# Kernel optimization log

Hardware: AMD Instinct MI355X
Metric: run time of the kernel (lower is better)

Reference implementation:

```python
import jax, jax.numpy as jnp
import numpy as np

B, S, E, WIN = 8, 2048, 512, 11  # batch, seq_len, emb_dim, window_size (odd)
PAD_VAL = 0.0  # padding_idx used as constant pad value in F.pad


def setup_inputs() -> dict:
    key = jax.random.key(0)
    k1, k2, k3 = jax.random.split(key, 3)
    x = jax.random.normal(k1, (B, S, E), dtype=jnp.float32)
    lim = 1.0 / np.sqrt(E * WIN)  # torch Linear default init bound
    # One independent Linear per timestep (deepcopy clones): stacked weights/bias
    W = jax.random.uniform(k2, (S, WIN, WIN * E), minval=-lim, maxval=lim, dtype=jnp.float32)
    b = jax.random.uniform(k3, (S, WIN), minval=-lim, maxval=lim, dtype=jnp.float32)
    return {"x": x, "W": W, "b": b}


def reference(x, W, b):
    ww = WIN // 2
    # pad sequence dim on both sides with padding_idx
    padded = jnp.pad(x, ((0, 0), (ww, ww), (0, 0)), constant_values=PAD_VAL)  # [B, S+2ww, E]
    # gather all sliding windows at once: windows[b,t,j,:] = padded[b, t+j, :]
    idx = jnp.arange(S)[:, None] + jnp.arange(WIN)[None, :]
    windows = padded[:, idx, :]
    flat = windows.reshape(B, S, WIN * E)                     # flattened window per position
    gates = jax.nn.sigmoid(jnp.einsum('bsf,swf->bsw', flat, W) + b)
    # gate * embeddings, sum over window, tanh
    score = jnp.einsum('bsw,bswe->bse', gates, windows)       # [B, S, E]
    return jnp.tanh(score)
```

## Files before the change

kernel.cpp:

```cpp
#include <hip/hip_runtime.h>
#include <math.h>

#define B_    8
#define S_    2048
#define E_    512
#define WIN_  11
#define WW    5
#define F4C   1408
#define E4C   128
#define PSTR  (B_ * WIN_)
#define HC_W  704
#define HC_X  512

template <int CTRL, int RMASK>
__device__ __forceinline__ float dpp_add(float v) {
    int sh = __builtin_amdgcn_update_dpp(0, __float_as_int(v),
                                         CTRL, RMASK, 0xF, true);
    return v + __int_as_float(sh);
}
__device__ __forceinline__ float wave_sum63(float v) {
    v = dpp_add<0x111, 0xF>(v);
    v = dpp_add<0x112, 0xF>(v);
    v = dpp_add<0x114, 0xF>(v);
    v = dpp_add<0x118, 0xF>(v);
    v = dpp_add<0x142, 0xA>(v);
    v = dpp_add<0x143, 0xC>(v);
    return v;
}

__device__ __forceinline__ float tanh_fast(float v) {
    const float e = __expf(v + v);
    return 1.f - 2.f / (e + 1.f);
}

__global__ __launch_bounds__(256)
void win_attn_fused(const float* __restrict__ x,
                    const float* __restrict__ W,
                    const float* __restrict__ bias,
                    float* __restrict__ out)
{
    const int bid  = blockIdx.x;
    const int s    = (bid & 7) * (S_ / 8) + (bid >> 3);
    const int tid  = threadIdx.x;
    const int wid  = tid >> 6;
    const int lane = tid & 63;

    const float4* __restrict__ X4 = reinterpret_cast<const float4*>(x);
    const float4* __restrict__ Ws = reinterpret_cast<const float4*>(W)
                                    + (size_t)s * (WIN_ * F4C);

    __shared__ float4 Wb[2][HC_W];
    __shared__ float4 xb[2][HC_X];
    __shared__ float gates[PSTR];

    const int w0   = wid * 3;
    const int wcnt = (wid == 3) ? 2 : 3;

    auto STAGE = [&](int buf, int c) {
        const int wp  = c >> 1;
        const int h   = c & 1;
        const int row = s - WW + wp;
        #pragma unroll
        for (int j = 0; j < 3; ++j) {
            const int m = j * 256 + tid;
            if (j < 2 || tid < 192) {
                const int w  = m >> 6;
                const int el = m & 63;
                const float4* src = Ws + (size_t)w * F4C + wp * E4C + h * 64 + el;
                __builtin_amdgcn_global_load_lds(
                    (const __attribute__((address_space(1))) void*)src,
                    (__attribute__((address_space(3))) void*)&Wb[buf][m],
                    16, 0, 0);
            }
        }
        #pragma unroll
        for (int j = 0; j < 2; ++j) {
            const int n  = j * 256 + tid;
            const int b  = n >> 6;
            const int el = n & 63;
            const float4* src = X4 + ((size_t)b * S_ + row) * E4C + h * 64 + el;
            __builtin_amdgcn_global_load_lds(
                (const __attribute__((address_space(1))) void*)src,
                (__attribute__((address_space(3))) void*)&xb[buf][n],
                16, 0, 0);
        }
    };

    float acc[B_][3];
    #pragma unroll
    for (int b = 0; b < B_; ++b)
        #pragma unroll
        for (int j = 0; j < 3; ++j) acc[b][j] = 0.f;

    const int wpLo = (s >= WW) ? 0 : (WW - s);
    const int wpHi = (WIN_ < S_ + WW - s) ? WIN_ : (S_ + WW - s);
    const int cLo  = 2 * wpLo, cHi = 2 * wpHi;

    STAGE(0, cLo);
    int cur = 0;

    #pragma unroll 1
    for (int c = cLo; c < cHi; ++c) {
        const bool more = (c + 1 < cHi);
        if (more) STAGE(cur ^ 1, c + 1);

        if (more) {
            if (wid < 3) asm volatile("s_waitcnt vmcnt(5)" ::: "memory");
            else         asm volatile("s_waitcnt vmcnt(4)" ::: "memory");
        } else {
            asm volatile("s_waitcnt vmcnt(0)" ::: "memory");
        }
        __builtin_amdgcn_s_barrier();
        __builtin_amdgcn_sched_barrier(0);

        float4 wv[3];
        #pragma unroll
        for (int j = 0; j < 3; ++j)
            if (j < wcnt) wv[j] = Wb[cur][(w0 + j) * 64 + lane];

        float4 xv[B_];
        #pragma unroll
        for (int b = 0; b < B_; ++b) xv[b] = xb[cur][b * 64 + lane];

        #pragma unroll
        for (int b = 0; b < B_; ++b)
            #pragma unroll
            for (int j = 0; j < 3; ++j)
                if (j < wcnt) {
                    float a = acc[b][j];
                    a = fmaf(xv[b].x, wv[j].x, a);
                    a = fmaf(xv[b].y, wv[j].y, a);
                    a = fmaf(xv[b].z, wv[j].z, a);
                    a = fmaf(xv[b].w, wv[j].w, a);
                    acc[b][j] = a;
                }

        __builtin_amdgcn_s_barrier();
        cur ^= 1;
    }

    #pragma unroll
    for (int b = 0; b < B_; ++b)
        #pragma unroll
        for (int j = 0; j < 3; ++j)
            if (j < wcnt) acc[b][j] = wave_sum63(acc[b][j]);

    if (lane == 63) {
        #pragma unroll
        for (int b = 0; b < B_; ++b)
            #pragma unroll
            for (int j = 0; j < 3; ++j)
                if (j < wcnt) gates[b * WIN_ + w0 + j] = acc[b][j];
    }
    __syncthreads();

    if (tid < PSTR) {
        const int w = tid % WIN_;
        const float v = gates[tid] + bias[s * WIN_ + w];
        gates[tid] = 1.f / (1.f + __expf(-v));
    }
    __syncthreads();

    float4* __restrict__ OUT4 = reinterpret_cast<float4*>(out);
    #pragma unroll
    for (int it = 0; it < 4; ++it) {
        const int i  = tid + (it << 8);
        const int b  = i >> 7;
        const int e4 = i & 127;
        float4 sc = make_float4(0.f, 0.f, 0.f, 0.f);
        #pragma unroll
        for (int w = 0; w < WIN_; ++w) {
            const int r = s - WW + w;
            if (r >= 0 && r < S_) {
                const float g   = gates[b * WIN_ + w];
                const float4 xv = X4[((size_t)b * S_ + r) * E4C + e4];
                sc.x = fmaf(g, xv.x, sc.x);
                sc.y = fmaf(g, xv.y, sc.y);
                sc.z = fmaf(g, xv.z, sc.z);
                sc.w = fmaf(g, xv.w, sc.w);
            }
        }
        float4 o;
        o.x = tanh_fast(sc.x);
        o.y = tanh_fast(sc.y);
        o.z = tanh_fast(sc.z);
        o.w = tanh_fast(sc.w);
        OUT4[((size_t)b * S_ + s) * E4C + e4] = o;
    }
}

extern "C" void kernel_launch(void* const* d_in, const int* in_sizes, int n_in,
                              void* d_out, int out_size, void* d_ws, size_t ws_size,
                              hipStream_t stream)
{
    const float* x    = (const float*)d_in[0];
    const float* W    = (const float*)d_in[1];
    const float* bias = (const float*)d_in[2];
    float* out        = (float*)d_out;

    win_attn_fused<<<dim3(S_), dim3(256), 0, stream>>>(x, W, bias, out);
}
```

Before: 146.6 us.

## Process two timesteps per block to share staged window rows of x

Each block now handles two adjacent sequence positions. It iterates over the 12 input rows covering both windows and loads each x row into LDS once, using it against both timesteps' weight slices. This halves the grid and cuts repeated x staging. In exchange it drops the double-buffered asynchronous pipeline with fine-grained vmcnt waits, and uses plain __syncthreads between loads and compute. That can expose load latency on the dominant W stream, whose traffic is unchanged.

```diff
diff --git a/kernel.cpp b/kernel.cpp
--- a/kernel.cpp
+++ b/kernel.cpp
@@ -8,9 +8,9 @@
 #define WW    5
 #define F4C   1408
 #define E4C   128
+#define G_    2
+#define NBLK  (S_ / G_)
 #define PSTR  (B_ * WIN_)
-#define HC_W  704
-#define HC_X  512
 
 template <int CTRL, int RMASK>
 __device__ __forceinline__ float dpp_add(float v) {
@@ -40,152 +40,189 @@
                     float* __restrict__ out)
 {
     const int bid  = blockIdx.x;
-    const int s    = (bid & 7) * (S_ / 8) + (bid >> 3);
+    const int sb   = (bid & 7) * (NBLK / 8) + (bid >> 3);
+    const int s0   = sb * G_;
     const int tid  = threadIdx.x;
     const int wid  = tid >> 6;
     const int lane = tid & 63;
 
-    const float4* __restrict__ X4 = reinterpret_cast<const float4*>(x);
-    const float4* __restrict__ Ws = reinterpret_cast<const float4*>(W)
-                                    + (size_t)s * (WIN_ * F4C);
-
-    __shared__ float4 Wb[2][HC_W];
-    __shared__ float4 xb[2][HC_X];
-    __shared__ float gates[PSTR];
+    const float4* __restrict__ X4  = reinterpret_cast<const float4*>(x);
+    const float4* __restrict__ Ws0 = reinterpret_cast<const float4*>(W)
+                                     + (size_t)s0 * (WIN_ * F4C);
+    const float4* __restrict__ Ws1 = Ws0 + (WIN_ * F4C);
+
+    __shared__ float4 xb[B_ * 64];
+    __shared__ float4 Wb0[WIN_ * 64];
+    __shared__ float4 Wb1[WIN_ * 64];
+    __shared__ float gates[G_ * PSTR];
 
     const int w0   = wid * 3;
     const int wcnt = (wid == 3) ? 2 : 3;
 
-    auto STAGE = [&](int buf, int c) {
-        const int wp  = c >> 1;
-        const int h   = c & 1;
-        const int row = s - WW + wp;
-        #pragma unroll
-        for (int j = 0; j < 3; ++j) {
-            const int m = j * 256 + tid;
-            if (j < 2 || tid < 192) {
-                const int w  = m >> 6;
-                const int el = m & 63;
-                const float4* src = Ws + (size_t)w * F4C + wp * E4C + h * 64 + el;
+    float acc[G_][B_][3];
+    #pragma unroll
+    for (int si = 0; si < G_; ++si)
+        #pragma unroll
+        for (int b = 0; b < B_; ++b)
+            #pragma unroll
+            for (int j = 0; j < 3; ++j) acc[si][b][j] = 0.f;
+
+    #pragma unroll 1
+    for (int r = s0 - WW; r <= s0 + WW + 1; ++r) {
+        if (r < 0 || r >= S_) continue;
+        const int wp0 = r - s0 + WW;
+        const int wp1 = wp0 - 1;
+        const bool v0 = (wp0 <= WIN_ - 1);
+        const bool v1 = (wp1 >= 0);
+
+        #pragma unroll
+        for (int h = 0; h < 2; ++h) {
+            #pragma unroll
+            for (int j = 0; j < 2; ++j) {
+                const int n  = j * 256 + tid;
+                const int b  = n >> 6;
+                const int el = n & 63;
+                const float4* src = X4 + ((size_t)b * S_ + r) * E4C + h * 64 + el;
                 __builtin_amdgcn_global_load_lds(
                     (const __attribute__((address_space(1))) void*)src,
-                    (__attribute__((address_space(3))) void*)&Wb[buf][m],
+                    (__attribute__((address_space(3))) void*)&xb[n],
                     16, 0, 0);
             }
+            if (v0) {
+                #pragma unroll
+                for (int j = 0; j < 3; ++j) {
+                    const int m = j * 256 + tid;
+                    if (j < 2 || tid < 192) {
+                        const int w  = m >> 6;
+                        const int el = m & 63;
+                        const float4* src = Ws0 + (size_t)w * F4C
+                                            + wp0 * E4C + h * 64 + el;
+                        __builtin_amdgcn_global_load_lds(
+                            (const __attribute__((address_space(1))) void*)src,
+                            (__attribute__((address_space(3))) void*)&Wb0[m],
+                            16, 0, 0);
+                    }
+                }
+            }
+            if (v1) {
+                #pragma unroll
+                for (int j = 0; j < 3; ++j) {
+                    const int m = j * 256 + tid;
+                    if (j < 2 || tid < 192) {
+                        const int w  = m >> 6;
+                        const int el = m & 63;
+                        const float4* src = Ws1 + (size_t)w * F4C
+                                            + wp1 * E4C + h * 64 + el;
+                        __builtin_amdgcn_global_load_lds(
+                            (const __attribute__((address_space(1))) void*)src,
+                            (__attribute__((address_space(3))) void*)&Wb1[m],
+                            16, 0, 0);
+                    }
+                }
+            }
+            __syncthreads();
+
+            float4 xv[B_];
+            #pragma unroll
+            for (int b = 0; b < B_; ++b) xv[b] = xb[b * 64 + lane];
+
+            if (v0) {
+                float4 wv[3];
+                #pragma unroll
+                for (int j = 0; j < 3; ++j)
+                    if (j < wcnt) wv[j] = Wb0[(w0 + j) * 64 + lane];
+                #pragma unroll
+                for (int b = 0; b < B_; ++b)
+                    #pragma unroll
+                    for (int j = 0; j < 3; ++j)
+                        if (j < wcnt) {
+                            float a = acc[0][b][j];
+                            a = fmaf(xv[b].x, wv[j].x, a);
+                            a = fmaf(xv[b].y, wv[j].y, a);
+                            a = fmaf(xv[b].z, wv[j].z, a);
+                            a = fmaf(xv[b].w, wv[j].w, a);
+                            acc[0][b][j] = a;
+                        }
+            }
+            if (v1) {
+                float4 wv[3];
+                #pragma unroll
+                for (int j = 0; j < 3; ++j)
+                    if (j < wcnt) wv[j] = Wb1[(w0 + j) * 64 + lane];
+                #pragma unroll
+                for (int b = 0; b < B_; ++b)
+                    #pragma unroll
+                    for (int j = 0; j < 3; ++j)
+                        if (j < wcnt) {
+                            float a = acc[1][b][j];
+                            a = fmaf(xv[b].x, wv[j].x, a);
+                            a = fmaf(xv[b].y, wv[j].y, a);
+                            a = fmaf(xv[b].z, wv[j].z, a);
+                            a = fmaf(xv[b].w, wv[j].w, a);
+                            acc[1][b][j] = a;
+                        }
+            }
+            __syncthreads();
         }
-        #pragma unroll
-        for (int j = 0; j < 2; ++j) {
-            const int n  = j * 256 + tid;
-            const int b  = n >> 6;
-            const int el = n & 63;
-            const float4* src = X4 + ((size_t)b * S_ + row) * E4C + h * 64 + el;
-            __builtin_amdgcn_global_load_lds(
-                (const __attribute__((address_space(1))) void*)src,
-                (__attribute__((address_space(3))) void*)&xb[buf][n],
-                16, 0, 0);
-        }
-    };
-
-    float acc[B_][3];
+    }
+
     #pragma unroll
-    for (int b = 0; b < B_; ++b)
-        #pragma unroll
-        for (int j = 0; j < 3; ++j) acc[b][j] = 0.f;
-
-    const int wpLo = (s >= WW) ? 0 : (WW - s);
-    const int wpHi = (WIN_ < S_ + WW - s) ? WIN_ : (S_ + WW - s);
-    const int cLo  = 2 * wpLo, cHi = 2 * wpHi;
-
-    STAGE(0, cLo);
-    int cur = 0;
-
-    #pragma unroll 1
-    for (int c = cLo; c < cHi; ++c) {
-        const bool more = (c + 1 < cHi);
-        if (more) STAGE(cur ^ 1, c + 1);
-
-        if (more) {
-            if (wid < 3) asm volatile("s_waitcnt vmcnt(5)" ::: "memory");
-            else         asm volatile("s_waitcnt vmcnt(4)" ::: "memory");
-        } else {
-            asm volatile("s_waitcnt vmcnt(0)" ::: "memory");
-        }
-        __builtin_amdgcn_s_barrier();
-        __builtin_amdgcn_sched_barrier(0);
-
-        float4 wv[3];
-        #pragma unroll
-        for (int j = 0; j < 3; ++j)
-            if (j < wcnt) wv[j] = Wb[cur][(w0 + j) * 64 + lane];
-
-        float4 xv[B_];
-        #pragma unroll
-        for (int b = 0; b < B_; ++b) xv[b] = xb[cur][b * 64 + lane];
-
+    for (int si = 0; si < G_; ++si)
         #pragma unroll
         for (int b = 0; b < B_; ++b)
             #pragma unroll
             for (int j = 0; j < 3; ++j)
-                if (j < wcnt) {
-                    float a = acc[b][j];
-                    a = fmaf(xv[b].x, wv[j].x, a);
-                    a = fmaf(xv[b].y, wv[j].y, a);
-                    a = fmaf(xv[b].z, wv[j].z, a);
-                    a = fmaf(xv[b].w, wv[j].w, a);
-                    acc[b][j] = a;
-                }
-
-        __builtin_amdgcn_s_barrier();
-        cur ^= 1;
-    }
-
-    #pragma unroll
-    for (int b = 0; b < B_; ++b)
-        #pragma unroll
-        for (int j = 0; j < 3; ++j)
-            if (j < wcnt) acc[b][j] = wave_sum63(acc[b][j]);
+                if (j < wcnt) acc[si][b][j] = wave_sum63(acc[si][b][j]);
 
     if (lane == 63) {
         #pragma unroll
-        for (int b = 0; b < B_; ++b)
-            #pragma unroll
-            for (int j = 0; j < 3; ++j)
-                if (j < wcnt) gates[b * WIN_ + w0 + j] = acc[b][j];
+        for (int si = 0; si < G_; ++si)
+            #pragma unroll
+            for (int b = 0; b < B_; ++b)
+                #pragma unroll
+                for (int j = 0; j < 3; ++j)
+                    if (j < wcnt)
+                        gates[si * PSTR + b * WIN_ + w0 + j] = acc[si][b][j];
     }
     __syncthreads();
 
-    if (tid < PSTR) {
-        const int w = tid % WIN_;
-        const float v = gates[tid] + bias[s * WIN_ + w];
+    if (tid < G_ * PSTR) {
+        const int si = tid / PSTR;
+        const int w  = tid % WIN_;
+        const float v = gates[tid] + bias[(s0 + si) * WIN_ + w];
         gates[tid] = 1.f / (1.f + __expf(-v));
     }
     __syncthreads();
 
     float4* __restrict__ OUT4 = reinterpret_cast<float4*>(out);
     #pragma unroll
-    for (int it = 0; it < 4; ++it) {
-        const int i  = tid + (it << 8);
-        const int b  = i >> 7;
-        const int e4 = i & 127;
-        float4 sc = make_float4(0.f, 0.f, 0.f, 0.f);
-        #pragma unroll
-        for (int w = 0; w < WIN_; ++w) {
-            const int r = s - WW + w;
-            if (r >= 0 && r < S_) {
-                const float g   = gates[b * WIN_ + w];
-                const float4 xv = X4[((size_t)b * S_ + r) * E4C + e4];
-                sc.x = fmaf(g, xv.x, sc.x);
-                sc.y = fmaf(g, xv.y, sc.y);
-                sc.z = fmaf(g, xv.z, sc.z);
-                sc.w = fmaf(g, xv.w, sc.w);
-            }
+    for (int si = 0; si < G_; ++si) {
+        const int s = s0 + si;
+        #pragma unroll
+        for (int it = 0; it < 4; ++it) {
+            const int i  = tid + (it << 8);
+            const int b  = i >> 7;
+            const int e4 = i & 127;
+            float4 sc = make_float4(0.f, 0.f, 0.f, 0.f);
+            #pragma unroll
+            for (int w = 0; w < WIN_; ++w) {
+                const int rr = s - WW + w;
+                if (rr >= 0 && rr < S_) {
+                    const float g   = gates[si * PSTR + b * WIN_ + w];
+                    const float4 xv = X4[((size_t)b * S_ + rr) * E4C + e4];
+                    sc.x = fmaf(g, xv.x, sc.x);
+                    sc.y = fmaf(g, xv.y, sc.y);
+                    sc.z = fmaf(g, xv.z, sc.z);
+                    sc.w = fmaf(g, xv.w, sc.w);
+                }
+            }
+            float4 o;
+            o.x = tanh_fast(sc.x);
+            o.y = tanh_fast(sc.y);
+            o.z = tanh_fast(sc.z);
+            o.w = tanh_fast(sc.w);
+            OUT4[((size_t)b * S_ + s) * E4C + e4] = o;
         }
-        float4 o;
-        o.x = tanh_fast(sc.x);
-        o.y = tanh_fast(sc.y);
-        o.z = tanh_fast(sc.z);
-        o.w = tanh_fast(sc.w);
-        OUT4[((size_t)b * S_ + s) * E4C + e4] = o;
     }
 }
 
@@ -198,5 +235,5 @@
     const float* bias = (const float*)d_in[2];
     float* out        = (float*)d_out;
 
-    win_attn_fused<<<dim3(S_), dim3(256), 0, stream>>>(x, W, bias, out);
-}
+    win_attn_fused<<<dim3(NBLK), dim3(256), 0, stream>>>(x, W, bias, out);
+}
```

Measured after the change: 155.1 us. +5.8%, slower.

## Drop double-buffered LDS staging in favor of single buffer with nontemporal W loads

Applied to the files above, without the earlier changes.

Replaces the double-buffered async global-to-LDS pipeline with a single buffer: each chunk is loaded, then the block syncs, computes and syncs again. The weight loads also get a cache-policy bit (aux=2), likely marking them streaming or nontemporal since W is read only once. This halves LDS use, which could raise occupancy, and simplifies the waitcnt logic, but it gives up overlap of loads with compute inside a block.

```diff
diff --git a/kernel.cpp b/kernel.cpp
--- a/kernel.cpp
+++ b/kernel.cpp
@@ -9,8 +9,6 @@
 #define F4C   1408
 #define E4C   128
 #define PSTR  (B_ * WIN_)
-#define HC_W  704
-#define HC_X  512
 
 template <int CTRL, int RMASK>
 __device__ __forceinline__ float dpp_add(float v) {
@@ -49,17 +47,28 @@
     const float4* __restrict__ Ws = reinterpret_cast<const float4*>(W)
                                     + (size_t)s * (WIN_ * F4C);
 
-    __shared__ float4 Wb[2][HC_W];
-    __shared__ float4 xb[2][HC_X];
+    __shared__ float4 Wb[WIN_ * 64];
+    __shared__ float4 xb[B_ * 64];
     __shared__ float gates[PSTR];
 
     const int w0   = wid * 3;
     const int wcnt = (wid == 3) ? 2 : 3;
 
-    auto STAGE = [&](int buf, int c) {
+    float acc[B_][3];
+    #pragma unroll
+    for (int b = 0; b < B_; ++b)
+        #pragma unroll
+        for (int j = 0; j < 3; ++j) acc[b][j] = 0.f;
+
+    const int wpLo = (s >= WW) ? 0 : (WW - s);
+    const int wpHi = (WIN_ < S_ + WW - s) ? WIN_ : (S_ + WW - s);
+
+    #pragma unroll 1
+    for (int c = 2 * wpLo; c < 2 * wpHi; ++c) {
         const int wp  = c >> 1;
         const int h   = c & 1;
         const int row = s - WW + wp;
+
         #pragma unroll
         for (int j = 0; j < 3; ++j) {
             const int m = j * 256 + tid;
@@ -69,8 +78,8 @@
                 const float4* src = Ws + (size_t)w * F4C + wp * E4C + h * 64 + el;
                 __builtin_amdgcn_global_load_lds(
                     (const __attribute__((address_space(1))) void*)src,
-                    (__attribute__((address_space(3))) void*)&Wb[buf][m],
-                    16, 0, 0);
+                    (__attribute__((address_space(3))) void*)&Wb[m],
+                    16, 0, 2 );
             }
         }
         #pragma unroll
@@ -81,46 +90,19 @@
             const float4* src = X4 + ((size_t)b * S_ + row) * E4C + h * 64 + el;
             __builtin_amdgcn_global_load_lds(
                 (const __attribute__((address_space(1))) void*)src,
-                (__attribute__((address_space(3))) void*)&xb[buf][n],
+                (__attribute__((address_space(3))) void*)&xb[n],
                 16, 0, 0);
         }
-    };
-
-    float acc[B_][3];
-    #pragma unroll
-    for (int b = 0; b < B_; ++b)
-        #pragma unroll
-        for (int j = 0; j < 3; ++j) acc[b][j] = 0.f;
-
-    const int wpLo = (s >= WW) ? 0 : (WW - s);
-    const int wpHi = (WIN_ < S_ + WW - s) ? WIN_ : (S_ + WW - s);
-    const int cLo  = 2 * wpLo, cHi = 2 * wpHi;
-
-    STAGE(0, cLo);
-    int cur = 0;
-
-    #pragma unroll 1
-    for (int c = cLo; c < cHi; ++c) {
-        const bool more = (c + 1 < cHi);
-        if (more) STAGE(cur ^ 1, c + 1);
-
-        if (more) {
-            if (wid < 3) asm volatile("s_waitcnt vmcnt(5)" ::: "memory");
-            else         asm volatile("s_waitcnt vmcnt(4)" ::: "memory");
-        } else {
-            asm volatile("s_waitcnt vmcnt(0)" ::: "memory");
-        }
-        __builtin_amdgcn_s_barrier();
-        __builtin_amdgcn_sched_barrier(0);
+        __syncthreads();
 
         float4 wv[3];
         #pragma unroll
         for (int j = 0; j < 3; ++j)
-            if (j < wcnt) wv[j] = Wb[cur][(w0 + j) * 64 + lane];
+            if (j < wcnt) wv[j] = Wb[(w0 + j) * 64 + lane];
 
         float4 xv[B_];
         #pragma unroll
-        for (int b = 0; b < B_; ++b) xv[b] = xb[cur][b * 64 + lane];
+        for (int b = 0; b < B_; ++b) xv[b] = xb[b * 64 + lane];
 
         #pragma unroll
         for (int b = 0; b < B_; ++b)
@@ -135,8 +117,7 @@
                     acc[b][j] = a;
                 }
 
-        __builtin_amdgcn_s_barrier();
-        cur ^= 1;
+        __syncthreads();
     }
 
     #pragma unroll
```

Result: faster. 129.7 us (-11.5%).

## Shrink block to single wave computing all window gates without barriers

Applied to the files above, without the earlier changes.

Each block now runs one 64-thread wave instead of four. That single wave stages all 11 W rows and 8 x rows per chunk and accumulates all 88 batch-by-window dot products in registers. The inter-wave s_barrier pairs in the chunk loop go away, leaving only vmcnt waits, and the W loads use a cache-policy flag. In exchange each wave holds many more accumulator registers and issues 19 async loads per stage. Each block also has four times fewer threads for the gather/tanh epilogue and for hiding memory latency.

```diff
diff --git a/kernel.cpp b/kernel.cpp
--- a/kernel.cpp
+++ b/kernel.cpp
@@ -9,8 +9,6 @@
 #define F4C   1408
 #define E4C   128
 #define PSTR  (B_ * WIN_)
-#define HC_W  704
-#define HC_X  512
 
 template <int CTRL, int RMASK>
 __device__ __forceinline__ float dpp_add(float v) {
@@ -33,7 +31,7 @@
     return 1.f - 2.f / (e + 1.f);
 }
 
-__global__ __launch_bounds__(256)
+__global__ __launch_bounds__(64)
 void win_attn_fused(const float* __restrict__ x,
                     const float* __restrict__ W,
                     const float* __restrict__ bias,
@@ -41,56 +39,43 @@
 {
     const int bid  = blockIdx.x;
     const int s    = (bid & 7) * (S_ / 8) + (bid >> 3);
-    const int tid  = threadIdx.x;
-    const int wid  = tid >> 6;
-    const int lane = tid & 63;
+    const int lane = threadIdx.x;
 
     const float4* __restrict__ X4 = reinterpret_cast<const float4*>(x);
     const float4* __restrict__ Ws = reinterpret_cast<const float4*>(W)
                                     + (size_t)s * (WIN_ * F4C);
 
-    __shared__ float4 Wb[2][HC_W];
-    __shared__ float4 xb[2][HC_X];
+    __shared__ float4 Wb[2][WIN_ * 64];
+    __shared__ float4 xb[2][B_ * 64];
     __shared__ float gates[PSTR];
-
-    const int w0   = wid * 3;
-    const int wcnt = (wid == 3) ? 2 : 3;
 
     auto STAGE = [&](int buf, int c) {
         const int wp  = c >> 1;
         const int h   = c & 1;
         const int row = s - WW + wp;
         #pragma unroll
-        for (int j = 0; j < 3; ++j) {
-            const int m = j * 256 + tid;
-            if (j < 2 || tid < 192) {
-                const int w  = m >> 6;
-                const int el = m & 63;
-                const float4* src = Ws + (size_t)w * F4C + wp * E4C + h * 64 + el;
-                __builtin_amdgcn_global_load_lds(
-                    (const __attribute__((address_space(1))) void*)src,
-                    (__attribute__((address_space(3))) void*)&Wb[buf][m],
-                    16, 0, 0);
-            }
+        for (int j = 0; j < WIN_; ++j) {
+            const float4* src = Ws + (size_t)j * F4C + wp * E4C + h * 64 + lane;
+            __builtin_amdgcn_global_load_lds(
+                (const __attribute__((address_space(1))) void*)src,
+                (__attribute__((address_space(3))) void*)&Wb[buf][j * 64],
+                16, 0, 2 );
         }
         #pragma unroll
-        for (int j = 0; j < 2; ++j) {
-            const int n  = j * 256 + tid;
-            const int b  = n >> 6;
-            const int el = n & 63;
-            const float4* src = X4 + ((size_t)b * S_ + row) * E4C + h * 64 + el;
+        for (int j = 0; j < B_; ++j) {
+            const float4* src = X4 + ((size_t)j * S_ + row) * E4C + h * 64 + lane;
             __builtin_amdgcn_global_load_lds(
                 (const __attribute__((address_space(1))) void*)src,
-                (__attribute__((address_space(3))) void*)&xb[buf][n],
+                (__attribute__((address_space(3))) void*)&xb[buf][j * 64],
                 16, 0, 0);
         }
     };
 
-    float acc[B_][3];
+    float acc[B_][WIN_];
     #pragma unroll
     for (int b = 0; b < B_; ++b)
         #pragma unroll
-        for (int j = 0; j < 3; ++j) acc[b][j] = 0.f;
+        for (int w = 0; w < WIN_; ++w) acc[b][w] = 0.f;
 
     const int wpLo = (s >= WW) ? 0 : (WW - s);
     const int wpHi = (WIN_ < S_ + WW - s) ? WIN_ : (S_ + WW - s);
@@ -104,67 +89,61 @@
         const bool more = (c + 1 < cHi);
         if (more) STAGE(cur ^ 1, c + 1);
 
-        if (more) {
-            if (wid < 3) asm volatile("s_waitcnt vmcnt(5)" ::: "memory");
-            else         asm volatile("s_waitcnt vmcnt(4)" ::: "memory");
-        } else {
-            asm volatile("s_waitcnt vmcnt(0)" ::: "memory");
-        }
-        __builtin_amdgcn_s_barrier();
+        if (more) asm volatile("s_waitcnt vmcnt(19)" ::: "memory");
+        else      asm volatile("s_waitcnt vmcnt(0)"  ::: "memory");
         __builtin_amdgcn_sched_barrier(0);
-
-        float4 wv[3];
-        #pragma unroll
-        for (int j = 0; j < 3; ++j)
-            if (j < wcnt) wv[j] = Wb[cur][(w0 + j) * 64 + lane];
 
         float4 xv[B_];
         #pragma unroll
         for (int b = 0; b < B_; ++b) xv[b] = xb[cur][b * 64 + lane];
 
         #pragma unroll
-        for (int b = 0; b < B_; ++b)
+        for (int w = 0; w < WIN_; ++w) {
+            const float4 wv = Wb[cur][w * 64 + lane];
             #pragma unroll
-            for (int j = 0; j < 3; ++j)
-                if (j < wcnt) {
-                    float a = acc[b][j];
-                    a = fmaf(xv[b].x, wv[j].x, a);
-                    a = fmaf(xv[b].y, wv[j].y, a);
-                    a = fmaf(xv[b].z, wv[j].z, a);
-                    a = fmaf(xv[b].w, wv[j].w, a);
-                    acc[b][j] = a;
-                }
-
-        __builtin_amdgcn_s_barrier();
+            for (int b = 0; b < B_; ++b) {
+                float a = acc[b][w];
+                a = fmaf(xv[b].x, wv.x, a);
+                a = fmaf(xv[b].y, wv.y, a);
+                a = fmaf(xv[b].z, wv.z, a);
+                a = fmaf(xv[b].w, wv.w, a);
+                acc[b][w] = a;
+            }
+        }
+        __builtin_amdgcn_sched_barrier(0);
         cur ^= 1;
     }
 
     #pragma unroll
     for (int b = 0; b < B_; ++b)
         #pragma unroll
-        for (int j = 0; j < 3; ++j)
-            if (j < wcnt) acc[b][j] = wave_sum63(acc[b][j]);
+        for (int w = 0; w < WIN_; ++w)
+            acc[b][w] = wave_sum63(acc[b][w]);
 
     if (lane == 63) {
         #pragma unroll
         for (int b = 0; b < B_; ++b)
             #pragma unroll
-            for (int j = 0; j < 3; ++j)
-                if (j < wcnt) gates[b * WIN_ + w0 + j] = acc[b][j];
+            for (int w = 0; w < WIN_; ++w)
+                gates[b * WIN_ + w] = acc[b][w];
     }
     __syncthreads();
 
-    if (tid < PSTR) {
-        const int w = tid % WIN_;
-        const float v = gates[tid] + bias[s * WIN_ + w];
-        gates[tid] = 1.f / (1.f + __expf(-v));
+    #pragma unroll
+    for (int rep = 0; rep < 2; ++rep) {
+        const int i = rep * 64 + lane;
+        if (i < PSTR) {
+            const int w = i % WIN_;
+            const float v = gates[i] + bias[s * WIN_ + w];
+            gates[i] = 1.f / (1.f + __expf(-v));
+        }
     }
     __syncthreads();
 
     float4* __restrict__ OUT4 = reinterpret_cast<float4*>(out);
     #pragma unroll
-    for (int it = 0; it < 4; ++it) {
-        const int i  = tid + (it << 8);
+    for (int it = 0; it < 16; ++it) {
+        const int i  = it * 64 + lane;
         const int b  = i >> 7;
         const int e4 = i & 127;
         float4 sc = make_float4(0.f, 0.f, 0.f, 0.f);
@@ -198,5 +177,5 @@
     const float* bias = (const float*)d_in[2];
     float* out        = (float*)d_out;
 
-    win_attn_fused<<<dim3(S_), dim3(256), 0, stream>>>(x, W, bias, out);
+    win_attn_fused<<<dim3(S_), dim3(64), 0, stream>>>(x, W, bias, out);
 }
```

Result: no change. 149.0 us (+1.6%).
